# Performance work log

Hardware: AMD Instinct MI355X
Metric: run time of the kernel (lower is better)

Reference implementation:

```python
import jax, jax.numpy as jnp
import numpy as np
from jax import lax

B, T, D = 16, 800, 80
HOP = 256          # hop_size
WIN = 512          # window_size = 2*hop
FFT = 1024         # fft_size
CCH = 256          # conv_channels
OUT = 222          # ltv_out_channels
GRP = 8            # group_size


def _conv1d_same(h, W, b, groups=1):
    # h: (B, C, T); W: (O, C//groups, 3). torch Conv1d pads (k-1)*d=2 then slices
    # [pad//2 : -pad//2], which is exactly SAME padding (1,1) for k=3, d=1.
    y = lax.conv_general_dilated(h, W, (1,), [(1, 1)], feature_group_count=groups,
                                 dimension_numbers=('NCH', 'OIH', 'NCH'))
    return y + b[None, :, None]


def setup_inputs() -> dict:
    key = jax.random.key(0)
    ks = jax.random.split(key, 8)
    s = 0.02  # small weight scale keeps 10**(Re(FFT)/10) numerically sane
    x = jax.random.normal(ks[0], (B, T, D), jnp.float32)
    z = 0.1 * jax.random.normal(ks[1], (B, 1, T * HOP), jnp.float32)
    W1 = s * jax.random.normal(ks[2], (CCH, D, 3), jnp.float32)
    b1 = jnp.zeros((CCH,), jnp.float32)
    W2 = s * jax.random.normal(ks[3], (CCH, CCH // GRP, 3), jnp.float32)
    b2 = jnp.zeros((CCH,), jnp.float32)
    W3 = s * jax.random.normal(ks[4], (CCH, CCH // GRP, 3), jnp.float32)
    b3 = jnp.zeros((CCH,), jnp.float32)
    W4 = s * jax.random.normal(ks[5], (OUT, CCH, 3), jnp.float32)
    b4 = jnp.zeros((OUT,), jnp.float32)
    return dict(x=x, z=z, W1=W1, b1=b1, W2=W2, b2=b2, W3=W3, b3=b3, W4=W4, b4=b4)


def _forward(x, z, W1, b1, W2, b2, W3, b3, W4, b4):
    # --- ConvLayers (original_conv): conv/relu stack over time axis ---
    h = x.transpose(0, 2, 1)                          # (B, D, T)
    h = jax.nn.relu(_conv1d_same(h, W1, b1))
    h = jax.nn.relu(_conv1d_same(h, W2, b2, GRP))
    h = jax.nn.relu(_conv1d_same(h, W3, b3, GRP))
    ccep = _conv1d_same(h, W4, b4).transpose(0, 2, 1)  # (B, T, 222)
    # quefrency norm: [111,...,1, 1,...,111]
    idx = jnp.arange(1, OUT // 2 + 1, dtype=ccep.dtype)
    quef = jnp.concatenate([idx[::-1], idx])
    ccep = ccep / quef

    # --- _ccep2impulse: cepstrum -> impulse response via FFT ---
    pad = (FFT - OUT) // 2                            # 401
    Y = jnp.fft.fft(jnp.pad(ccep, ((0, 0), (0, 0), (pad, pad))), n=FFT, axis=-1)
    mag = 10.0 ** (Y.real / 10.0)
    imp = jnp.fft.ifft(mag * jnp.exp(1j * Y.imag), n=FFT, axis=-1).real  # (B,T,1024)

    # --- _conv_impulse: per-frame time-varying convolution ---
    zp = jnp.pad(z.reshape(B, -1), ((0, 0), (WIN // 2 - 1, WIN // 2)))   # (B, L+511)
    fidx = jnp.arange(T)[:, None] * HOP + jnp.arange(WIN)[None, :]
    frames = zp[:, fidx]                                                 # (B, T, 512)
    fp = jnp.pad(frames, ((0, 0), (0, 0), (FFT // 2 - 1, FFT // 2)))     # (B, T, 1535)
    # out[n] = sum_k fp[n+k] * imp[k]  (valid cross-correlation, 512 outputs).
    # Realize as circular correlation with N=2048 >= 1534+512 (no wraparound).
    N = 2048
    C = jnp.fft.irfft(jnp.fft.rfft(fp, N) * jnp.conj(jnp.fft.rfft(imp, N)), N)[..., :WIN]

    # --- _ola: window + overlap-add ---
    n = jnp.arange(WIN, dtype=C.dtype)
    win = 0.5 * (1.0 - jnp.cos(2.0 * jnp.pi * n / WIN))  # periodic hann, win_norm=1
    zw = C * win                                          # (B, T, 512)
    ola = zw[..., :HOP] + jnp.roll(zw[..., HOP:], 1, axis=1)
    return jnp.clip(ola.reshape(B, 1, T * HOP), -1.0, 1.0)


def reference(x, z, W1, b1, W2, b2, W3, b3, W4, b4):
    return _forward(x, z, W1, b1, W2, b2, W3, b3, W4, b4)
```

## Files before the change

### kernel.cpp

```cpp
#include <hip/hip_runtime.h>
#include <hip/hip_bf16.h>

#define T_LEN 800
#define B_SZ  16
#define D_IN  80
#define CCH   256
#define OUT_CH 222
#define HOPSZ 256
#define WINSZ 512
#define ZLEN  (T_LEN*HOPSZ)
#define CSTRIDE 256
#define XSTR 104

#define PHI(i) ((i) + ((i)>>3))

typedef short short8 __attribute__((ext_vector_type(8)));
typedef float f32x4 __attribute__((ext_vector_type(4)));

__device__ __forceinline__ float2 cmul(float2 a, float2 b){
    return make_float2(a.x*b.x - a.y*b.y, a.x*b.y + a.y*b.x);
}

__global__ __launch_bounds__(256) void k_wtrans(const float* __restrict__ W1,
                                                const float* __restrict__ W2,
                                                const float* __restrict__ W3,
                                                const float* __restrict__ W4,
                                                float4* __restrict__ w2t,
                                                float4* __restrict__ w3t,
                                                __hip_bfloat16* __restrict__ w1fhi,
                                                __hip_bfloat16* __restrict__ w1flo,
                                                __hip_bfloat16* __restrict__ wfhi,
                                                __hip_bfloat16* __restrict__ wflo){
    const int i = blockIdx.x*256 + threadIdx.x;
    switch (blockIdx.y){
    case 0: if (i < 32*256){
        int cil = i >> 8, co = i & 255;
        const float* s = &W2[(co*32 + cil)*3];
        w2t[i] = make_float4(s[0], s[1], s[2], 0.f);
    } break;
    case 1: if (i < 32*256){
        int cil = i >> 8, co = i & 255;
        const float* s = &W3[(co*32 + cil)*3];
        w3t[i] = make_float4(s[0], s[1], s[2], 0.f);
    } break;
    case 2: if (i < 9*4*256*8){
        int e  = i & 7;
        int co = (i >> 3) & 255;
        int lg = (i >> 11) & 3;
        int dk = i >> 13;
        int d  = dk / 3, kt = dk - 3*d;
        int ci = kt*32 + lg*8 + e;
        float w = (ci < 80) ? W1[(co*80 + ci)*3 + d] : 0.f;
        __hip_bfloat16 h = __float2bfloat16(w);
        __hip_bfloat16 l = __float2bfloat16(w - __bfloat162float(h));
        w1fhi[i] = h;
        w1flo[i] = l;
    } break;
    default: if (i < 768*256){
        int k = i >> 8, co = i & 255;
        int d = k >> 8, ci = k & 255;
        float w = 0.f;
        if (co < OUT_CH){
            float q = (co < 111) ? (float)(111 - co) : (float)(co - 110);
            w = W4[(co*256 + ci)*3 + d] / q;
        }
        __hip_bfloat16 h = __float2bfloat16(w);
        __hip_bfloat16 l = __float2bfloat16(w - __bfloat162float(h));
        int kt = k >> 5, g = (k >> 3) & 3, e = k & 7;
        int idx = ((kt*4 + g)*256 + co)*8 + e;
        wfhi[idx] = h;
        wflo[idx] = l;
    } break;
    }
}

__global__ __launch_bounds__(256) void k_conv123(const float* __restrict__ x,
                                                 const __hip_bfloat16* __restrict__ w1fhi,
                                                 const __hip_bfloat16* __restrict__ w1flo,
                                                 const float* __restrict__ b1,
                                                 const float4* __restrict__ W2t,
                                                 const float* __restrict__ b2,
                                                 const float4* __restrict__ W3t,
                                                 const float* __restrict__ b3,
                                                 __hip_bfloat16* __restrict__ ohi,
                                                 __hip_bfloat16* __restrict__ olo){
    __shared__ __align__(16) __hip_bfloat16 xhi[34*XSTR];
    __shared__ __align__(16) __hip_bfloat16 xlo[34*XSTR];
    __shared__ __align__(16) float hs[256*20];
    const int t0 = blockIdx.x * 16;
    const int b  = blockIdx.y;
    const int tid = threadIdx.x;
    const int co = tid;
    const int gbase = (co >> 5) << 5;
    const int wave = tid >> 6;
    const int l = tid & 63;
    const int l15 = l & 15, lg4 = l >> 4;

    for (int i = tid; i < 34*XSTR; i += 256){
        int rr = i / XSTR, c = i - rr*XSTR;
        float v = 0.f;
        if (c < 80){
            int t = t0 - 3 + rr;
            v = (t >= 0 && t < T_LEN) ? x[(b*T_LEN + t)*D_IN + c] : 0.f;
        }
        __hip_bfloat16 h = __float2bfloat16(v);
        xhi[i] = h;
        xlo[i] = __float2bfloat16(v - __bfloat162float(h));
    }
    __syncthreads();

    {
        f32x4 acc1[2][4];
        #pragma unroll
        for (int n = 0; n < 4; ++n){
            float bv = b1[(wave << 6) + (n << 4) + l15];
            acc1[0][n] = f32x4{bv, bv, bv, bv};
            acc1[1][n] = f32x4{bv, bv, bv, bv};
        }
        #pragma unroll
        for (int d = 0; d < 3; ++d){
            #pragma unroll
            for (int kt = 0; kt < 3; ++kt){
                short8 ah[2], al[2];
                #pragma unroll
                for (int m = 0; m < 2; ++m){
                    int off = ((m << 4) + l15 + d)*XSTR + kt*32 + lg4*8;
                    ah[m] = __builtin_bit_cast(short8, *(const uint4*)(xhi + off));
                    al[m] = __builtin_bit_cast(short8, *(const uint4*)(xlo + off));
                }
                #pragma unroll
                for (int n = 0; n < 4; ++n){
                    int co_n = (wave << 6) + (n << 4) + l15;
                    int wo = ((((d*3 + kt)*4 + lg4) << 8) + co_n) << 3;
                    short8 bh = __builtin_bit_cast(short8, *(const uint4*)(w1fhi + wo));
                    short8 bl = __builtin_bit_cast(short8, *(const uint4*)(w1flo + wo));
                    #pragma unroll
                    for (int m = 0; m < 2; ++m){
                        acc1[m][n] = __builtin_amdgcn_mfma_f32_16x16x32_bf16(ah[m], bh, acc1[m][n], 0, 0, 0);
                        acc1[m][n] = __builtin_amdgcn_mfma_f32_16x16x32_bf16(ah[m], bl, acc1[m][n], 0, 0, 0);
                        acc1[m][n] = __builtin_amdgcn_mfma_f32_16x16x32_bf16(al[m], bh, acc1[m][n], 0, 0, 0);
                    }
                }
            }
        }
        #pragma unroll
        for (int m = 0; m < 2; ++m){
            #pragma unroll
            for (int n = 0; n < 4; ++n){
                int co_n = (wave << 6) + (n << 4) + l15;
                #pragma unroll
                for (int j = 0; j < 4; ++j){
                    int trow = (m << 4) + (lg4 << 2) + j;
                    if (trow < 20){
                        int t = t0 - 2 + trow;
                        float v = (t >= 0 && t < T_LEN) ? fmaxf(acc1[m][n][j], 0.f) : 0.f;
                        hs[co_n*20 + trow] = v;
                    }
                }
            }
        }
    }
    __syncthreads();

    float acc2[18];
    {
        float bv = b2[co];
        #pragma unroll
        for (int j = 0; j < 18; ++j) acc2[j] = bv;
        const float4* wp = W2t + co;
        float4 w = *wp;
        for (int cil = 0; cil < 32; ++cil){
            wp += 256;
            float4 wn = *wp;
            const float* xp = &hs[(gbase + cil)*20];
            float4 v0 = *(const float4*)(xp);
            float4 v1 = *(const float4*)(xp + 4);
            float4 v2 = *(const float4*)(xp + 8);
            float4 v3 = *(const float4*)(xp + 12);
            float4 v4 = *(const float4*)(xp + 16);
            float xr[20] = {v0.x,v0.y,v0.z,v0.w, v1.x,v1.y,v1.z,v1.w,
                            v2.x,v2.y,v2.z,v2.w, v3.x,v3.y,v3.z,v3.w,
                            v4.x,v4.y,v4.z,v4.w};
            #pragma unroll
            for (int j = 0; j < 18; ++j){
                acc2[j] = fmaf(xr[j],   w.x, acc2[j]);
                acc2[j] = fmaf(xr[j+1], w.y, acc2[j]);
                acc2[j] = fmaf(xr[j+2], w.z, acc2[j]);
            }
            w = wn;
        }
    }
    __syncthreads();
    #pragma unroll
    for (int j = 0; j < 18; ++j){
        int t = t0 - 1 + j;
        hs[co*20 + j] = (t >= 0 && t < T_LEN) ? fmaxf(acc2[j], 0.f) : 0.f;
    }
    __syncthreads();
    float acc3[16];
    {
        float bv = b3[co];
        #pragma unroll
        for (int j = 0; j < 16; ++j) acc3[j] = bv;
        const float4* wp = W3t + co;
        float4 w = *wp;
        for (int cil = 0; cil < 32; ++cil){
            wp += 256;
            float4 wn = *wp;
            const float* xp = &hs[(gbase + cil)*20];
            float4 v0 = *(const float4*)(xp);
            float4 v1 = *(const float4*)(xp + 4);
            float4 v2 = *(const float4*)(xp + 8);
            float4 v3 = *(const float4*)(xp + 12);
            float2 v4 = *(const float2*)(xp + 16);
            float xr[18] = {v0.x,v0.y,v0.z,v0.w, v1.x,v1.y,v1.z,v1.w,
                            v2.x,v2.y,v2.z,v2.w, v3.x,v3.y,v3.z,v3.w, v4.x,v4.y};
            #pragma unroll
            for (int j = 0; j < 16; ++j){
                acc3[j] = fmaf(xr[j],   w.x, acc3[j]);
                acc3[j] = fmaf(xr[j+1], w.y, acc3[j]);
                acc3[j] = fmaf(xr[j+2], w.z, acc3[j]);
            }
            w = wn;
        }
    }
    #pragma unroll
    for (int j = 0; j < 16; ++j){
        float v = fmaxf(acc3[j], 0.f);
        __hip_bfloat16 h = __float2bfloat16(v);
        __hip_bfloat16 l = __float2bfloat16(v - __bfloat162float(h));
        size_t idx = (size_t)(b*T_LEN + t0 + j)*CCH + co;
        ohi[idx] = h;
        olo[idx] = l;
    }
}

__global__ __launch_bounds__(256) void k_conv4(const __hip_bfloat16* __restrict__ hhi,
                                               const __hip_bfloat16* __restrict__ hlo,
                                               const __hip_bfloat16* __restrict__ wfhi,
                                               const __hip_bfloat16* __restrict__ wflo,
                                               const float* __restrict__ bias,
                                               float* __restrict__ ccep){
    __shared__ __align__(16) unsigned char aLds[2][34*512];
    const int gx = blockIdx.x;
    const int b  = gx / 25;
    const int t0 = (gx - b*25) * 32;
    const int coBase = blockIdx.y << 7;
    const int tid = threadIdx.x;
    const int wave = tid >> 6;
    const int l = tid & 63;
    const int l15 = l & 15, lg = l >> 4;

    for (int i = tid; i < 2*1088; i += 256){
        int p = (i >= 1088);
        int c = i - (p ? 1088 : 0);
        int r = c >> 5, c16 = c & 31;
        int t = t0 - 1 + r;
        uint4 v = make_uint4(0u,0u,0u,0u);
        if (t >= 0 && t < T_LEN){
            const __hip_bfloat16* src = (p ? hlo : hhi) + (((size_t)(b*T_LEN + t)) << 8) + (c16 << 3);
            v = *(const uint4*)src;
        }
        int off = (r << 9) + (c16 << 4);
        off ^= (r & 7) << 4;
        *(uint4*)(&aLds[p][off]) = v;
    }
    __syncthreads();

    const int co0 = coBase + (wave << 5);
    f32x4 acc[2][2];
    #pragma unroll
    for (int n = 0; n < 2; ++n){
        int co = co0 + (n << 4) + l15;
        float bq = 0.f;
        if (co < OUT_CH){
            float q = (co < 111) ? (float)(111 - co) : (float)(co - 110);
            bq = bias[co] / q;
        }
        acc[0][n] = f32x4{bq, bq, bq, bq};
        acc[1][n] = f32x4{bq, bq, bq, bq};
    }

    for (int kt = 0; kt < 24; ++kt){
        const int d   = kt >> 3;
        const int cib = (kt & 7) << 6;
        short8 ah[2], al[2];
        #pragma unroll
        for (int m = 0; m < 2; ++m){
            int r = l15 + d + (m << 4);
            int off = (r << 9) + cib + (lg << 4);
            off ^= (r & 7) << 4;
            ah[m] = __builtin_bit_cast(short8, *(const uint4*)(&aLds[0][off]));
            al[m] = __builtin_bit_cast(short8, *(const uint4*)(&aLds[1][off]));
        }
        #pragma unroll
        for (int n = 0; n < 2; ++n){
            int co = co0 + (n << 4) + l15;
            size_t woff = ((size_t)((kt << 2) + lg) << 8) + co;
            short8 bh = __builtin_bit_cast(short8, *(const uint4*)(wfhi + (woff << 3)));
            short8 bl = __builtin_bit_cast(short8, *(const uint4*)(wflo + (woff << 3)));
            #pragma unroll
            for (int m = 0; m < 2; ++m){
                acc[m][n] = __builtin_amdgcn_mfma_f32_16x16x32_bf16(ah[m], bh, acc[m][n], 0, 0, 0);
                acc[m][n] = __builtin_amdgcn_mfma_f32_16x16x32_bf16(ah[m], bl, acc[m][n], 0, 0, 0);
                acc[m][n] = __builtin_amdgcn_mfma_f32_16x16x32_bf16(al[m], bh, acc[m][n], 0, 0, 0);
            }
        }
    }

    #pragma unroll
    for (int m = 0; m < 2; ++m){
        #pragma unroll
        for (int n = 0; n < 2; ++n){
            int co = co0 + (n << 4) + l15;
            #pragma unroll
            for (int j = 0; j < 4; ++j){
                int t = t0 + (m << 4) + (lg << 2) + j;
                ccep[((size_t)(b*T_LEN + t) << 8) + co] = acc[m][n][j];
            }
        }
    }
}

template<int N4, int Ns, bool INV, bool SKIP3>
__device__ __forceinline__ void r4s(const float2* __restrict__ src,
                                    float2* __restrict__ dst,
                                    const float2* __restrict__ Wt,
                                    int j){
    const int jm = j & (Ns - 1);
    float2 v0 = src[PHI(j)];
    float2 v1 = src[PHI(j + N4)];
    float2 v2 = src[PHI(j + 2*N4)];
    float2 v3 = make_float2(0.f, 0.f);
    if (!SKIP3) v3 = src[PHI(j + 3*N4)];
    if (Ns > 1){
        const int e = jm * (256 / Ns);
        float2 w1 = Wt[PHI(e)];
        if (INV) w1.y = -w1.y;
        float2 w2 = cmul(w1, w1);
        float2 w3 = cmul(w2, w1);
        v1 = cmul(v1, w1);
        v2 = cmul(v2, w2);
        if (!SKIP3) v3 = cmul(v3, w3);
    }
    float2 t0 = make_float2(v0.x + v2.x, v0.y + v2.y);
    float2 t1 = make_float2(v0.x - v2.x, v0.y - v2.y);
    float2 t2, t3;
    if (SKIP3){ t2 = v1; t3 = v1; }
    else {
        t2 = make_float2(v1.x + v3.x, v1.y + v3.y);
        t3 = make_float2(v1.x - v3.x, v1.y - v3.y);
    }
    float2 o0 = make_float2(t0.x + t2.x, t0.y + t2.y);
    float2 o2 = make_float2(t0.x - t2.x, t0.y - t2.y);
    float2 o1, o3;
    if (!INV){
        o1 = make_float2(t1.x + t3.y, t1.y - t3.x);
        o3 = make_float2(t1.x - t3.y, t1.y + t3.x);
    } else {
        o1 = make_float2(t1.x - t3.y, t1.y + t3.x);
        o3 = make_float2(t1.x + t3.y, t1.y - t3.x);
    }
    const int base = ((j - jm) << 2) + jm;
    dst[PHI(base)]          = o0;
    dst[PHI(base + Ns)]     = o1;
    dst[PHI(base + 2*Ns)]   = o2;
    dst[PHI(base + 3*Ns)]   = o3;
}

__global__ __launch_bounds__(256) void k_filter(const float* __restrict__ ccep,
                                                const float* __restrict__ z,
                                                float* __restrict__ zw){
    __shared__ __align__(16) float2 A[1152];
    __shared__ __align__(16) float2 Bb[1152];
    __shared__ __align__(16) float2 Wt[576];
    const int t = blockIdx.x;
    const int b = blockIdx.y;
    const int tid = threadIdx.x;
    const float PI2 = 6.283185307179586f;

    for (int j = tid; j < 512; j += 256){
        float s, c;
        __sincosf(-PI2 * (float)j * (1.0f/1024.0f), &s, &c);
        Wt[PHI(j)] = make_float2(c, s);
    }
    {
        const float* crow = &ccep[(b*T_LEN + t)*CSTRIDE];
        auto gen = [&](int i)->float2 {
            float av = (i >= 401 && i < 623) ? crow[i - 401] : 0.f;
            float fv = 0.f;
            if (i < 512){
                int zi = t*HOPSZ + i - 255;
                fv = (zi >= 0 && zi < ZLEN) ? z[b*ZLEN + zi] : 0.f;
            }
            return make_float2(av, fv);
        };
        int j = tid;
        float2 v0 = gen(j);
        float2 v1 = gen(j + 256);
        float2 v2 = gen(j + 512);
        float2 t0 = make_float2(v0.x + v2.x, v0.y + v2.y);
        float2 t1 = make_float2(v0.x - v2.x, v0.y - v2.y);
        int base = PHI(4*j);
        Bb[base]     = make_float2(t0.x + v1.x, t0.y + v1.y);
        Bb[base + 1] = make_float2(t1.x + v1.y, t1.y - v1.x);
        Bb[base + 2] = make_float2(t0.x - v1.x, t0.y - v1.y);
        Bb[base + 3] = make_float2(t1.x - v1.y, t1.y + v1.x);
    }
    __syncthreads();

    r4s<256,4,  false,false>(Bb, A,  Wt, tid); __syncthreads();
    r4s<256,16, false,false>(A,  Bb, Wt, tid); __syncthreads();
    r4s<256,64, false,false>(Bb, A,  Wt, tid); __syncthreads();
    r4s<256,256,false,false>(A,  Bb, Wt, tid); __syncthreads();

    {
        const float LOG2_10_DIV10 = 0.33219280948873623f;
        auto unpackG = [&](int i)->float2 {
            float2 P = Bb[PHI(i)];
            float2 Q = Bb[PHI((1024 - i) & 1023)];
            float Are = 0.5f * (P.x + Q.x);
            float Aim = 0.5f * (P.y - Q.y);
            float Fx  = 0.5f * (P.y + Q.y);
            float Fy  = 0.5f * (Q.x - P.x);
            float mag = exp2f(Are * LOG2_10_DIV10) * (1.0f/1024.0f);
            float s, c;
            __sincosf(Aim, &s, &c);
            float Hx = mag * c, Hy = mag * s;
            return make_float2(Fx*Hx + Fy*Hy, Fx*Hy - Fy*Hx);
        };
        int k = tid;
        float2 G  = unpackG(k);
        float2 G2 = unpackG(512 - k);
        float sx = G.x + G2.x, sy = G.y - G2.y;
        float dx = G.x - G2.x, dy = G.y + G2.y;
        float2 V = Wt[PHI(k)];
        float ux = dx*V.x + dy*V.y;
        float uy = dy*V.x - dx*V.y;
        A[PHI(k)] = make_float2(sx - uy, sy + ux);
        if (k){
            A[PHI(512 - k)] = make_float2(sx + uy, ux - sy);
        } else {
            float2 G3 = unpackG(256);
            A[PHI(256)] = make_float2(2.f*G3.x, -2.f*G3.y);
        }
    }
    __syncthreads();

    if (tid < 128) r4s<128,1, true,false>(A,  Bb, Wt, tid);
    __syncthreads();
    if (tid < 128) r4s<128,4, true,false>(Bb, A,  Wt, tid);
    __syncthreads();
    if (tid < 128) r4s<128,16,true,false>(A,  Bb, Wt, tid);
    __syncthreads();
    if (tid < 128) r4s<128,64,true,false>(Bb, A,  Wt, tid);
    __syncthreads();

    {
        int j = tid;
        float2 u = A[PHI(j)];
        float2 v = A[PHI(j + 256)];
        float2 w = Wt[PHI(2*j)];
        w.y = -w.y;
        float2 vv = cmul(v, w);
        float zx = u.x + vv.x, zy = u.y + vv.y;
        int n1 = 511 - 2*j;
        int n2 = 510 - 2*j;
        float wv1 = 0.5f * (1.0f - __cosf(PI2 * (float)n1 * (1.0f/512.0f)));
        float wv2 = 0.5f * (1.0f - __cosf(PI2 * (float)n2 * (1.0f/512.0f)));
        float* zrow = &zw[(size_t)(b*T_LEN + t)*512];
        zrow[n1] = zx * wv1;
        zrow[n2] = zy * wv2;
    }
}

__global__ __launch_bounds__(256) void k_ola(const float* __restrict__ zw,
                                             float* __restrict__ out){
    const int t = blockIdx.x;
    const int b = blockIdx.y;
    const int h = threadIdx.x;
    const int tm = (t + T_LEN - 1) % T_LEN;
    float v = zw[(size_t)(b*T_LEN + t)*512 + h]
            + zw[(size_t)(b*T_LEN + tm)*512 + 256 + h];
    v = fminf(fmaxf(v, -1.0f), 1.0f);
    out[(size_t)b*ZLEN + t*HOPSZ + h] = v;
}

extern "C" void kernel_launch(void* const* d_in, const int* in_sizes, int n_in,
                              void* d_out, int out_size, void* d_ws, size_t ws_size,
                              hipStream_t stream){
    const float* x  = (const float*)d_in[0];
    const float* z  = (const float*)d_in[1];
    const float* W1 = (const float*)d_in[2];
    const float* b1 = (const float*)d_in[3];
    const float* W2 = (const float*)d_in[4];
    const float* b2 = (const float*)d_in[5];
    const float* W3 = (const float*)d_in[6];
    const float* b3 = (const float*)d_in[7];
    const float* W4 = (const float*)d_in[8];
    const float* b4 = (const float*)d_in[9];
    float* out = (float*)d_out;
    float* ws  = (float*)d_ws;

    float* ccep = ws;
    __hip_bfloat16* h3hi = (__hip_bfloat16*)(ws + 3276800);
    __hip_bfloat16* h3lo = h3hi + 3276800;
    float* zwb  = ws + 6553600;
    float4* w2t = (float4*)(zwb);
    float4* w3t = (float4*)(zwb + 32768);
    __hip_bfloat16* w1fhi = (__hip_bfloat16*)(zwb + 65536);
    __hip_bfloat16* w1flo = (__hip_bfloat16*)(zwb + 102400);
    __hip_bfloat16* wfhi  = (__hip_bfloat16*)(zwb + 139264);
    __hip_bfloat16* wflo  = (__hip_bfloat16*)(zwb + 237568);

    dim3 blk(256);
    dim3 gwt(768, 4);
    dim3 gconv(T_LEN/16, B_SZ);
    dim3 gc4(400, 2);
    dim3 gf(T_LEN, B_SZ);

    k_wtrans<<<gwt, blk, 0, stream>>>(W1, W2, W3, W4, w2t, w3t, w1fhi, w1flo, wfhi, wflo);
    k_conv123<<<gconv, blk, 0, stream>>>(x, w1fhi, w1flo, b1, w2t, b2, w3t, b3, h3hi, h3lo);
    k_conv4<<<gc4, blk, 0, stream>>>(h3hi, h3lo, wfhi, wflo, b4, ccep);
    k_filter<<<gf, blk, 0, stream>>>(ccep, z, zwb);
    k_ola<<<gf, blk, 0, stream>>>(zwb, out);
}
```

Before: 140.7 us.

## Move grouped conv2/conv3 to split-bf16 MFMA in separate kernel from conv1

Splits the fused conv1-3 kernel in two. Conv1 runs over 32-step tiles and writes its output to global memory as split hi/lo bf16. A new kernel computes the grouped conv2 and conv3 with three-term bf16 MFMA, using swizzled LDS tiles and weights pre-packed for MFMA, replacing the scalar fp32 FMA loops. This trades the compute-bound scalar grouped convolutions for an extra global round trip of the intermediate activation and one more kernel launch.

```diff
diff --git a/kernel.cpp b/kernel.cpp
--- a/kernel.cpp
+++ b/kernel.cpp
@@ -25,23 +25,43 @@
                                                 const float* __restrict__ W2,
                                                 const float* __restrict__ W3,
                                                 const float* __restrict__ W4,
-                                                float4* __restrict__ w2t,
-                                                float4* __restrict__ w3t,
                                                 __hip_bfloat16* __restrict__ w1fhi,
                                                 __hip_bfloat16* __restrict__ w1flo,
+                                                __hip_bfloat16* __restrict__ w2fhi,
+                                                __hip_bfloat16* __restrict__ w2flo,
+                                                __hip_bfloat16* __restrict__ w3fhi,
+                                                __hip_bfloat16* __restrict__ w3flo,
                                                 __hip_bfloat16* __restrict__ wfhi,
                                                 __hip_bfloat16* __restrict__ wflo){
     const int i = blockIdx.x*256 + threadIdx.x;
     switch (blockIdx.y){
-    case 0: if (i < 32*256){
-        int cil = i >> 8, co = i & 255;
-        const float* s = &W2[(co*32 + cil)*3];
-        w2t[i] = make_float4(s[0], s[1], s[2], 0.f);
+    case 0: if (i < 16*3*4*16*8){
+        int e   = i & 7;
+        int c15 = (i >> 3) & 15;
+        int lg  = (i >> 7) & 3;
+        int t   = i >> 9;
+        int d   = t % 3;
+        int gn  = t / 3;
+        int co  = (gn >> 1)*32 + (gn & 1)*16 + c15;
+        int cil = lg*8 + e;
+        float w = W2[(co*32 + cil)*3 + d];
+        __hip_bfloat16 h = __float2bfloat16(w);
+        w2fhi[i] = h;
+        w2flo[i] = __float2bfloat16(w - __bfloat162float(h));
     } break;
-    case 1: if (i < 32*256){
-        int cil = i >> 8, co = i & 255;
-        const float* s = &W3[(co*32 + cil)*3];
-        w3t[i] = make_float4(s[0], s[1], s[2], 0.f);
+    case 1: if (i < 16*3*4*16*8){
+        int e   = i & 7;
+        int c15 = (i >> 3) & 15;
+        int lg  = (i >> 7) & 3;
+        int t   = i >> 9;
+        int d   = t % 3;
+        int gn  = t / 3;
+        int co  = (gn >> 1)*32 + (gn & 1)*16 + c15;
+        int cil = lg*8 + e;
+        float w = W3[(co*32 + cil)*3 + d];
+        __hip_bfloat16 h = __float2bfloat16(w);
+        w3fhi[i] = h;
+        w3flo[i] = __float2bfloat16(w - __bfloat162float(h));
     } break;
     case 2: if (i < 9*4*256*8){
         int e  = i & 7;
@@ -52,9 +72,8 @@
         int ci = kt*32 + lg*8 + e;
         float w = (ci < 80) ? W1[(co*80 + ci)*3 + d] : 0.f;
         __hip_bfloat16 h = __float2bfloat16(w);
-        __hip_bfloat16 l = __float2bfloat16(w - __bfloat162float(h));
         w1fhi[i] = h;
-        w1flo[i] = l;
+        w1flo[i] = __float2bfloat16(w - __bfloat162float(h));
     } break;
     default: if (i < 768*256){
         int k = i >> 8, co = i & 255;
@@ -74,24 +93,17 @@
     }
 }
 
-__global__ __launch_bounds__(256) void k_conv123(const float* __restrict__ x,
-                                                 const __hip_bfloat16* __restrict__ w1fhi,
-                                                 const __hip_bfloat16* __restrict__ w1flo,
-                                                 const float* __restrict__ b1,
-                                                 const float4* __restrict__ W2t,
-                                                 const float* __restrict__ b2,
-                                                 const float4* __restrict__ W3t,
-                                                 const float* __restrict__ b3,
-                                                 __hip_bfloat16* __restrict__ ohi,
-                                                 __hip_bfloat16* __restrict__ olo){
+__global__ __launch_bounds__(256) void k_conv1m(const float* __restrict__ x,
+                                                const __hip_bfloat16* __restrict__ w1fhi,
+                                                const __hip_bfloat16* __restrict__ w1flo,
+                                                const float* __restrict__ b1,
+                                                __hip_bfloat16* __restrict__ ohi,
+                                                __hip_bfloat16* __restrict__ olo){
     __shared__ __align__(16) __hip_bfloat16 xhi[34*XSTR];
     __shared__ __align__(16) __hip_bfloat16 xlo[34*XSTR];
-    __shared__ __align__(16) float hs[256*20];
-    const int t0 = blockIdx.x * 16;
+    const int t0 = blockIdx.x * 32;
     const int b  = blockIdx.y;
     const int tid = threadIdx.x;
-    const int co = tid;
-    const int gbase = (co >> 5) << 5;
     const int wave = tid >> 6;
     const int l = tid & 63;
     const int l15 = l & 15, lg4 = l >> 4;
@@ -100,7 +112,7 @@
         int rr = i / XSTR, c = i - rr*XSTR;
         float v = 0.f;
         if (c < 80){
-            int t = t0 - 3 + rr;
+            int t = t0 - 1 + rr;
             v = (t >= 0 && t < T_LEN) ? x[(b*T_LEN + t)*D_IN + c] : 0.f;
         }
         __hip_bfloat16 h = __float2bfloat16(v);
@@ -109,129 +121,201 @@
     }
     __syncthreads();
 
-    {
-        f32x4 acc1[2][4];
-        #pragma unroll
-        for (int n = 0; n < 4; ++n){
-            float bv = b1[(wave << 6) + (n << 4) + l15];
-            acc1[0][n] = f32x4{bv, bv, bv, bv};
-            acc1[1][n] = f32x4{bv, bv, bv, bv};
-        }
-        #pragma unroll
-        for (int d = 0; d < 3; ++d){
-            #pragma unroll
-            for (int kt = 0; kt < 3; ++kt){
-                short8 ah[2], al[2];
+    f32x4 acc1[2][4];
+    #pragma unroll
+    for (int n = 0; n < 4; ++n){
+        float bv = b1[(wave << 6) + (n << 4) + l15];
+        acc1[0][n] = f32x4{bv, bv, bv, bv};
+        acc1[1][n] = f32x4{bv, bv, bv, bv};
+    }
+    #pragma unroll
+    for (int d = 0; d < 3; ++d){
+        #pragma unroll
+        for (int kt = 0; kt < 3; ++kt){
+            short8 ah[2], al[2];
+            #pragma unroll
+            for (int m = 0; m < 2; ++m){
+                int off = ((m << 4) + l15 + d)*XSTR + kt*32 + lg4*8;
+                ah[m] = __builtin_bit_cast(short8, *(const uint4*)(xhi + off));
+                al[m] = __builtin_bit_cast(short8, *(const uint4*)(xlo + off));
+            }
+            #pragma unroll
+            for (int n = 0; n < 4; ++n){
+                int co_n = (wave << 6) + (n << 4) + l15;
+                int wo = ((((d*3 + kt)*4 + lg4) << 8) + co_n) << 3;
+                short8 bh = __builtin_bit_cast(short8, *(const uint4*)(w1fhi + wo));
+                short8 bl = __builtin_bit_cast(short8, *(const uint4*)(w1flo + wo));
                 #pragma unroll
                 for (int m = 0; m < 2; ++m){
-                    int off = ((m << 4) + l15 + d)*XSTR + kt*32 + lg4*8;
-                    ah[m] = __builtin_bit_cast(short8, *(const uint4*)(xhi + off));
-                    al[m] = __builtin_bit_cast(short8, *(const uint4*)(xlo + off));
+                    acc1[m][n] = __builtin_amdgcn_mfma_f32_16x16x32_bf16(ah[m], bh, acc1[m][n], 0, 0, 0);
+                    acc1[m][n] = __builtin_amdgcn_mfma_f32_16x16x32_bf16(ah[m], bl, acc1[m][n], 0, 0, 0);
+                    acc1[m][n] = __builtin_amdgcn_mfma_f32_16x16x32_bf16(al[m], bh, acc1[m][n], 0, 0, 0);
                 }
+            }
+        }
+    }
+    #pragma unroll
+    for (int m = 0; m < 2; ++m){
+        #pragma unroll
+        for (int n = 0; n < 4; ++n){
+            int co_n = (wave << 6) + (n << 4) + l15;
+            #pragma unroll
+            for (int j = 0; j < 4; ++j){
+                int trow = (m << 4) + (lg4 << 2) + j;
+                float v = fmaxf(acc1[m][n][j], 0.f);
+                __hip_bfloat16 h = __float2bfloat16(v);
+                __hip_bfloat16 l2 = __float2bfloat16(v - __bfloat162float(h));
+                size_t idx = ((size_t)(b*T_LEN + t0 + trow) << 8) + co_n;
+                ohi[idx] = h;
+                olo[idx] = l2;
+            }
+        }
+    }
+}
+
+__global__ __launch_bounds__(256) void k_conv23(const __hip_bfloat16* __restrict__ hhi,
+                                                const __hip_bfloat16* __restrict__ hlo,
+                                                const __hip_bfloat16* __restrict__ w2fhi,
+                                                const __hip_bfloat16* __restrict__ w2flo,
+                                                const float* __restrict__ b2,
+                                                const __hip_bfloat16* __restrict__ w3fhi,
+                                                const __hip_bfloat16* __restrict__ w3flo,
+                                                const float* __restrict__ b3,
+                                                __hip_bfloat16* __restrict__ ohi,
+                                                __hip_bfloat16* __restrict__ olo){
+    __shared__ __align__(16) unsigned char inL[2][50*256];
+    __shared__ __align__(16) unsigned char imL[2][34*256];
+    const int t0 = blockIdx.x * 32;
+    const int b  = blockIdx.y;
+    const int coBase = blockIdx.z << 7;
+    const int tid = threadIdx.x;
+    const int gl = tid >> 6;
+    const int l = tid & 63;
+    const int l15 = l & 15, lg4 = l >> 4;
+    const int g = (coBase >> 5) + gl;
+
+    for (int i = tid; i < 2*800; i += 256){
+        int p = (i >= 800);
+        int c = i - (p ? 800 : 0);
+        int r = c >> 4, c16 = c & 15;
+        int t = t0 - 2 + r;
+        uint4 v = make_uint4(0u,0u,0u,0u);
+        if (t >= 0 && t < T_LEN){
+            const __hip_bfloat16* src = (p ? hlo : hhi) + (((size_t)(b*T_LEN + t)) << 8) + coBase + (c16 << 3);
+            v = *(const uint4*)src;
+        }
+        int off = (r << 8) + (c16 << 4);
+        off ^= (r & 7) << 4;
+        *(uint4*)(&inL[p][off]) = v;
+    }
+    __syncthreads();
+
+    {
+        f32x4 acc2[3][2];
+        #pragma unroll
+        for (int n = 0; n < 2; ++n){
+            float bv = b2[(g << 5) + (n << 4) + l15];
+            acc2[0][n] = f32x4{bv, bv, bv, bv};
+            acc2[1][n] = f32x4{bv, bv, bv, bv};
+            acc2[2][n] = f32x4{bv, bv, bv, bv};
+        }
+        #pragma unroll
+        for (int d = 0; d < 3; ++d){
+            short8 ah[3], al[3];
+            #pragma unroll
+            for (int m = 0; m < 3; ++m){
+                int rr = (m << 4) + l15 + d;
+                int off = (rr << 8) + (gl << 6) + (lg4 << 4);
+                off ^= (rr & 7) << 4;
+                ah[m] = __builtin_bit_cast(short8, *(const uint4*)(&inL[0][off]));
+                al[m] = __builtin_bit_cast(short8, *(const uint4*)(&inL[1][off]));
+            }
+            #pragma unroll
+            for (int n = 0; n < 2; ++n){
+                int wo = (((((g*2 + n)*3 + d)*4 + lg4) << 4) + l15) << 3;
+                short8 bh = __builtin_bit_cast(short8, *(const uint4*)(w2fhi + wo));
+                short8 bl = __builtin_bit_cast(short8, *(const uint4*)(w2flo + wo));
                 #pragma unroll
-                for (int n = 0; n < 4; ++n){
-                    int co_n = (wave << 6) + (n << 4) + l15;
-                    int wo = ((((d*3 + kt)*4 + lg4) << 8) + co_n) << 3;
-                    short8 bh = __builtin_bit_cast(short8, *(const uint4*)(w1fhi + wo));
-                    short8 bl = __builtin_bit_cast(short8, *(const uint4*)(w1flo + wo));
-                    #pragma unroll
-                    for (int m = 0; m < 2; ++m){
-                        acc1[m][n] = __builtin_amdgcn_mfma_f32_16x16x32_bf16(ah[m], bh, acc1[m][n], 0, 0, 0);
-                        acc1[m][n] = __builtin_amdgcn_mfma_f32_16x16x32_bf16(ah[m], bl, acc1[m][n], 0, 0, 0);
-                        acc1[m][n] = __builtin_amdgcn_mfma_f32_16x16x32_bf16(al[m], bh, acc1[m][n], 0, 0, 0);
+                for (int m = 0; m < 3; ++m){
+                    acc2[m][n] = __builtin_amdgcn_mfma_f32_16x16x32_bf16(ah[m], bh, acc2[m][n], 0, 0, 0);
+                    acc2[m][n] = __builtin_amdgcn_mfma_f32_16x16x32_bf16(ah[m], bl, acc2[m][n], 0, 0, 0);
+                    acc2[m][n] = __builtin_amdgcn_mfma_f32_16x16x32_bf16(al[m], bh, acc2[m][n], 0, 0, 0);
+                }
+            }
+        }
+        #pragma unroll
+        for (int m = 0; m < 3; ++m){
+            #pragma unroll
+            for (int n = 0; n < 2; ++n){
+                int cl2 = (gl << 5) + (n << 4) + l15;
+                #pragma unroll
+                for (int j = 0; j < 4; ++j){
+                    int orow = (m << 4) + (lg4 << 2) + j;
+                    if (orow < 34){
+                        int t = t0 - 1 + orow;
+                        float v = (t >= 0 && t < T_LEN) ? fmaxf(acc2[m][n][j], 0.f) : 0.f;
+                        __hip_bfloat16 h = __float2bfloat16(v);
+                        __hip_bfloat16 l2 = __float2bfloat16(v - __bfloat162float(h));
+                        int off = (orow << 8) + (cl2 << 1);
+                        off ^= (orow & 7) << 4;
+                        *(__hip_bfloat16*)(&imL[0][off]) = h;
+                        *(__hip_bfloat16*)(&imL[1][off]) = l2;
                     }
                 }
             }
         }
+    }
+    __syncthreads();
+
+    {
+        f32x4 acc3[2][2];
+        #pragma unroll
+        for (int n = 0; n < 2; ++n){
+            float bv = b3[(g << 5) + (n << 4) + l15];
+            acc3[0][n] = f32x4{bv, bv, bv, bv};
+            acc3[1][n] = f32x4{bv, bv, bv, bv};
+        }
+        #pragma unroll
+        for (int d = 0; d < 3; ++d){
+            short8 ah[2], al[2];
+            #pragma unroll
+            for (int m = 0; m < 2; ++m){
+                int rr = (m << 4) + l15 + d;
+                int off = (rr << 8) + (gl << 6) + (lg4 << 4);
+                off ^= (rr & 7) << 4;
+                ah[m] = __builtin_bit_cast(short8, *(const uint4*)(&imL[0][off]));
+                al[m] = __builtin_bit_cast(short8, *(const uint4*)(&imL[1][off]));
+            }
+            #pragma unroll
+            for (int n = 0; n < 2; ++n){
+                int wo = (((((g*2 + n)*3 + d)*4 + lg4) << 4) + l15) << 3;
+                short8 bh = __builtin_bit_cast(short8, *(const uint4*)(w3fhi + wo));
+                short8 bl = __builtin_bit_cast(short8, *(const uint4*)(w3flo + wo));
+                #pragma unroll
+                for (int m = 0; m < 2; ++m){
+                    acc3[m][n] = __builtin_amdgcn_mfma_f32_16x16x32_bf16(ah[m], bh, acc3[m][n], 0, 0, 0);
+                    acc3[m][n] = __builtin_amdgcn_mfma_f32_16x16x32_bf16(ah[m], bl, acc3[m][n], 0, 0, 0);
+                    acc3[m][n] = __builtin_amdgcn_mfma_f32_16x16x32_bf16(al[m], bh, acc3[m][n], 0, 0, 0);
+                }
+            }
+        }
         #pragma unroll
         for (int m = 0; m < 2; ++m){
             #pragma unroll
-            for (int n = 0; n < 4; ++n){
-                int co_n = (wave << 6) + (n << 4) + l15;
+            for (int n = 0; n < 2; ++n){
+                int co = coBase + (gl << 5) + (n << 4) + l15;
                 #pragma unroll
                 for (int j = 0; j < 4; ++j){
-                    int trow = (m << 4) + (lg4 << 2) + j;
-                    if (trow < 20){
-                        int t = t0 - 2 + trow;
-                        float v = (t >= 0 && t < T_LEN) ? fmaxf(acc1[m][n][j], 0.f) : 0.f;
-                        hs[co_n*20 + trow] = v;
-                    }
+                    int orow3 = (m << 4) + (lg4 << 2) + j;
+                    float v = fmaxf(acc3[m][n][j], 0.f);
+                    __hip_bfloat16 h = __float2bfloat16(v);
+                    __hip_bfloat16 l2 = __float2bfloat16(v - __bfloat162float(h));
+                    size_t idx = ((size_t)(b*T_LEN + t0 + orow3) << 8) + co;
+                    ohi[idx] = h;
+                    olo[idx] = l2;
                 }
             }
         }
-    }
-    __syncthreads();
-
-    float acc2[18];
-    {
-        float bv = b2[co];
-        #pragma unroll
-        for (int j = 0; j < 18; ++j) acc2[j] = bv;
-        const float4* wp = W2t + co;
-        float4 w = *wp;
-        for (int cil = 0; cil < 32; ++cil){
-            wp += 256;
-            float4 wn = *wp;
-            const float* xp = &hs[(gbase + cil)*20];
-            float4 v0 = *(const float4*)(xp);
-            float4 v1 = *(const float4*)(xp + 4);
-            float4 v2 = *(const float4*)(xp + 8);
-            float4 v3 = *(const float4*)(xp + 12);
-            float4 v4 = *(const float4*)(xp + 16);
-            float xr[20] = {v0.x,v0.y,v0.z,v0.w, v1.x,v1.y,v1.z,v1.w,
-                            v2.x,v2.y,v2.z,v2.w, v3.x,v3.y,v3.z,v3.w,
-                            v4.x,v4.y,v4.z,v4.w};
-            #pragma unroll
-            for (int j = 0; j < 18; ++j){
-                acc2[j] = fmaf(xr[j],   w.x, acc2[j]);
-                acc2[j] = fmaf(xr[j+1], w.y, acc2[j]);
-                acc2[j] = fmaf(xr[j+2], w.z, acc2[j]);
-            }
-            w = wn;
-        }
-    }
-    __syncthreads();
-    #pragma unroll
-    for (int j = 0; j < 18; ++j){
-        int t = t0 - 1 + j;
-        hs[co*20 + j] = (t >= 0 && t < T_LEN) ? fmaxf(acc2[j], 0.f) : 0.f;
-    }
-    __syncthreads();
-    float acc3[16];
-    {
-        float bv = b3[co];
-        #pragma unroll
-        for (int j = 0; j < 16; ++j) acc3[j] = bv;
-        const float4* wp = W3t + co;
-        float4 w = *wp;
-        for (int cil = 0; cil < 32; ++cil){
-            wp += 256;
-            float4 wn = *wp;
-            const float* xp = &hs[(gbase + cil)*20];
-            float4 v0 = *(const float4*)(xp);
-            float4 v1 = *(const float4*)(xp + 4);
-            float4 v2 = *(const float4*)(xp + 8);
-            float4 v3 = *(const float4*)(xp + 12);
-            float2 v4 = *(const float2*)(xp + 16);
-            float xr[18] = {v0.x,v0.y,v0.z,v0.w, v1.x,v1.y,v1.z,v1.w,
-                            v2.x,v2.y,v2.z,v2.w, v3.x,v3.y,v3.z,v3.w, v4.x,v4.y};
-            #pragma unroll
-            for (int j = 0; j < 16; ++j){
-                acc3[j] = fmaf(xr[j],   w.x, acc3[j]);
-                acc3[j] = fmaf(xr[j+1], w.y, acc3[j]);
-                acc3[j] = fmaf(xr[j+2], w.z, acc3[j]);
-            }
-            w = wn;
-        }
-    }
-    #pragma unroll
-    for (int j = 0; j < 16; ++j){
-        float v = fmaxf(acc3[j], 0.f);
-        __hip_bfloat16 h = __float2bfloat16(v);
-        __hip_bfloat16 l = __float2bfloat16(v - __bfloat162float(h));
-        size_t idx = (size_t)(b*T_LEN + t0 + j)*CCH + co;
-        ohi[idx] = h;
-        olo[idx] = l;
     }
 }
 
@@ -502,25 +586,32 @@
     float* out = (float*)d_out;
     float* ws  = (float*)d_ws;
 
+    __hip_bfloat16* h1hi = (__hip_bfloat16*)ws;
+    __hip_bfloat16* h1lo = h1hi + 3276800;
     float* ccep = ws;
     __hip_bfloat16* h3hi = (__hip_bfloat16*)(ws + 3276800);
     __hip_bfloat16* h3lo = h3hi + 3276800;
     float* zwb  = ws + 6553600;
-    float4* w2t = (float4*)(zwb);
-    float4* w3t = (float4*)(zwb + 32768);
-    __hip_bfloat16* w1fhi = (__hip_bfloat16*)(zwb + 65536);
-    __hip_bfloat16* w1flo = (__hip_bfloat16*)(zwb + 102400);
-    __hip_bfloat16* wfhi  = (__hip_bfloat16*)(zwb + 139264);
-    __hip_bfloat16* wflo  = (__hip_bfloat16*)(zwb + 237568);
+    __hip_bfloat16* w1fhi = (__hip_bfloat16*)zwb;
+    __hip_bfloat16* w1flo = w1fhi + 73728;
+    __hip_bfloat16* w2fhi = w1flo + 73728;
+    __hip_bfloat16* w2flo = w2fhi + 24576;
+    __hip_bfloat16* w3fhi = w2flo + 24576;
+    __hip_bfloat16* w3flo = w3fhi + 24576;
+    __hip_bfloat16* wfhi  = w3flo + 24576;
+    __hip_bfloat16* wflo  = wfhi + 196608;
 
     dim3 blk(256);
     dim3 gwt(768, 4);
-    dim3 gconv(T_LEN/16, B_SZ);
+    dim3 gc1(25, B_SZ);
+    dim3 gc23(25, B_SZ, 2);
     dim3 gc4(400, 2);
     dim3 gf(T_LEN, B_SZ);
 
-    k_wtrans<<<gwt, blk, 0, stream>>>(W1, W2, W3, W4, w2t, w3t, w1fhi, w1flo, wfhi, wflo);
-    k_conv123<<<gconv, blk, 0, stream>>>(x, w1fhi, w1flo, b1, w2t, b2, w3t, b3, h3hi, h3lo);
+    k_wtrans<<<gwt, blk, 0, stream>>>(W1, W2, W3, W4, w1fhi, w1flo, w2fhi, w2flo,
+                                      w3fhi, w3flo, wfhi, wflo);
+    k_conv1m<<<gc1, blk, 0, stream>>>(x, w1fhi, w1flo, b1, h1hi, h1lo);
+    k_conv23<<<gc23, blk, 0, stream>>>(h1hi, h1lo, w2fhi, w2flo, b2, w3fhi, w3flo, b3, h3hi, h3lo);
     k_conv4<<<gc4, blk, 0, stream>>>(h3hi, h3lo, wfhi, wflo, b4, ccep);
     k_filter<<<gf, blk, 0, stream>>>(ccep, z, zwb);
     k_ola<<<gf, blk, 0, stream>>>(zwb, out);
```

After: 126.5 us. -10.1%, faster.
